# Performance work log

Measured on AMD Instinct MI355X. Metric: run time of the kernel, lower is better.

## Reference

```python
import jax, jax.numpy as jnp
import numpy as np

# --- model config (matches init_kwargs) ---
T, R, L, H, D = 3, 4, 4, 8, 32      # node types, edge types, layers, heads, head dim
HID = H * D                          # hidden = 256
N, E = 16384, 65536                  # nodes per type, edges per edge type
REL = [(1, 0), (0, 2), (2, 1), (0, 0)]  # (src_type, dst_type) per edge type
EPS = 1e-5


def setup_inputs():
    key = jax.random.key(0)
    ks = jax.random.split(key, 24)
    w = lambda k, s: 0.05 * jax.random.normal(k, s, jnp.float32)
    d = {}
    for t in range(T):
        d[f"x{t}"] = jax.random.normal(ks[t], (N, HID), jnp.float32)
    for r in range(R):
        d[f"ei{r}"] = jax.random.randint(ks[3 + r], (2, E), 0, N)
    # input projections (per node type)
    d["Win"] = w(ks[10], (T, HID, HID)); d["b_in"] = jnp.zeros((T, HID), jnp.float32)
    # HGTConv per-layer, per-node-type k/q/v linears
    d["Kw"] = w(ks[11], (L, T, HID, HID)); d["Kb"] = jnp.zeros((L, T, HID), jnp.float32)
    d["Qw"] = w(ks[12], (L, T, HID, HID)); d["Qb"] = jnp.zeros((L, T, HID), jnp.float32)
    d["Vw"] = w(ks[13], (L, T, HID, HID)); d["Vb"] = jnp.zeros((L, T, HID), jnp.float32)
    # per-layer, per-edge-type relation matrices (key/message) and priority
    d["Arel"] = w(ks[14], (L, R, H, D, D)) + jnp.eye(D, dtype=jnp.float32)
    d["Mrel"] = w(ks[15], (L, R, H, D, D)) + jnp.eye(D, dtype=jnp.float32)
    d["Prel"] = jnp.ones((L, R, H), jnp.float32)
    # HGTConv output linear + learned skip gate, encoder LayerNorm
    d["Aw"] = w(ks[16], (L, T, HID, HID)); d["Ab"] = jnp.zeros((L, T, HID), jnp.float32)
    d["skip"] = jnp.ones((L, T), jnp.float32)
    d["ln_g"] = jnp.ones((L, T, HID), jnp.float32); d["ln_b"] = jnp.zeros((L, T, HID), jnp.float32)
    # output projections (per node type)
    d["Wout"] = w(ks[17], (T, HID, HID)); d["b_out"] = jnp.zeros((T, HID), jnp.float32)
    return d


def _layer_norm(y, g, b):
    mu = y.mean(-1, keepdims=True)
    var = ((y - mu) ** 2).mean(-1, keepdims=True)
    return (y - mu) * jax.lax.rsqrt(var + EPS) * g + b


def _hgt_forward(xs, eis, Win, b_in, Kw, Kb, Qw, Qb, Vw, Vb, Arel, Mrel, Prel,
                 Aw, Ab, skip, ln_g, ln_b, Wout, b_out):
    scale = 1.0 / np.sqrt(D).astype(np.float32)
    # input projections (dropout is identity in eval / p=0)
    hs = [xs[t] @ Win[t] + b_in[t] for t in range(T)]
    for l in range(L):
        k = [(hs[t] @ Kw[l, t] + Kb[l, t]).reshape(-1, H, D) for t in range(T)]
        q = [(hs[t] @ Qw[l, t] + Qb[l, t]).reshape(-1, H, D) for t in range(T)]
        v = [(hs[t] @ Vw[l, t] + Vb[l, t]).reshape(-1, H, D) for t in range(T)]
        # per-edge scores / messages, bucketed by destination node type
        sc_by = [[] for _ in range(T)]; mg_by = [[] for _ in range(T)]; di_by = [[] for _ in range(T)]
        for r, (s, dtp) in enumerate(REL):
            src, dst = eis[r][0], eis[r][1]
            k_rel = jnp.einsum('nhd,hde->nhe', k[s], Arel[l, r])  # relation-specific key transform
            m_rel = jnp.einsum('nhd,hde->nhe', v[s], Mrel[l, r])  # relation-specific message transform
            score = jnp.einsum('ehd,ehd->eh', q[dtp][dst], k_rel[src]) * Prel[l, r] * scale  # [E,H]
            sc_by[dtp].append(score); mg_by[dtp].append(m_rel[src]); di_by[dtp].append(dst)
        new_hs = []
        for t in range(T):
            sc = jnp.concatenate(sc_by[t], 0)       # [Et,H] scores over all incoming relations
            mg = jnp.concatenate(mg_by[t], 0)       # [Et,H,D]
            di = jnp.concatenate(di_by[t], 0)       # [Et]
            n = hs[t].shape[0]
            # segment softmax over each destination node's incoming edges (per head)
            mx = jax.ops.segment_max(sc, di, num_segments=n)
            ex = jnp.exp(sc - mx[di])
            den = jax.ops.segment_sum(ex, di, num_segments=n)
            alpha = ex / jnp.maximum(den[di], 1e-16)
            agg = jax.ops.segment_sum(mg * alpha[..., None], di, num_segments=n).reshape(n, HID)
            out = jax.nn.gelu(agg) @ Aw[l, t] + Ab[l, t]
            a = jax.nn.sigmoid(skip[l, t])
            conv = a * out + (1.0 - a) * hs[t]                    # HGTConv internal gated skip
            new_hs.append(_layer_norm(conv + hs[t], ln_g[l, t], ln_b[l, t]))  # encoder residual + LN
        hs = new_hs
    return tuple(hs[t] @ Wout[t] + b_out[t] for t in range(T))


def reference(x0, x1, x2, ei0, ei1, ei2, ei3, Win, b_in, Kw, Kb, Qw, Qb, Vw, Vb,
              Arel, Mrel, Prel, Aw, Ab, skip, ln_g, ln_b, Wout, b_out):
    return _hgt_forward([x0, x1, x2], [ei0, ei1, ei2, ei3], Win, b_in, Kw, Kb, Qw, Qb,
                        Vw, Vb, Arel, Mrel, Prel, Aw, Ab, skip, ln_g, ln_b, Wout, b_out)
```

## Files before the change

kernel.cpp:

```cpp
#include <hip/hip_runtime.h>

#define N_NODES 16384
#define E_EDGES 65536
#define HIDC 256
#define NM ((size_t)N_NODES * HIDC)
#define NSLOT 62
#define PLANEU ((size_t)NSLOT * 65536)
#define KMU ((size_t)N_NODES * 512)

typedef __attribute__((ext_vector_type(8))) short short8;
typedef __attribute__((ext_vector_type(4))) float f32x4;

__device__ __forceinline__ float gelu_f(float x) {
  return 0.5f * x * (1.0f + tanhf(0.7978845608028654f * (x + 0.044715f * x * x * x)));
}
__device__ __forceinline__ unsigned short bf16rne(float x) {
  unsigned u = __float_as_uint(x);
  return (unsigned short)((u + 0x7FFFu + ((u >> 16) & 1u)) >> 16);
}
__device__ __forceinline__ void split2(float x, unsigned short& h, unsigned short& l) {
  h = bf16rne(x);
  float rem = x - __uint_as_float(((unsigned)h) << 16);
  l = bf16rne(rem);
}
__device__ __forceinline__ float bf2f(unsigned short v) {
  return __uint_as_float(((unsigned)v) << 16);
}
__device__ __forceinline__ int src_of(int r) { return (r == 0) ? 1 : (r == 2) ? 2 : 0; }
__device__ __forceinline__ size_t woff(int k, int n) {
  return (size_t)(((n >> 6) & 3) * 16384 + (k >> 5) * 2048 + (((k >> 3) & 3) * 512) + ((n & 63) * 8) + (k & 7));
}
__device__ __forceinline__ size_t swz(int row, int k) {
  return ((size_t)(row >> 4) << 12) + ((size_t)(k >> 3) << 7) + ((row & 15) << 3) + (k & 7);
}

__device__ __forceinline__ void gemm_core(const unsigned short* __restrict__ Ahi,
                                          const unsigned short* __restrict__ Alo,
                                          const unsigned short* __restrict__ Whi,
                                          const unsigned short* __restrict__ Wlo,
                                          int bm, int ntt, f32x4 (&acc)[4][2]) {
  const int tid = threadIdx.x;
  const int w = tid >> 6, l = tid & 63;
  const int wm = (w >> 1) * 64, wn = (w & 1) * 32;
  const int lk = l >> 4, ln = l & 15;
  const size_t abase = ((size_t)((bm + wm) >> 4) << 12) + ln * 8;
  const size_t bbase = (size_t)ntt * 16384 + lk * 512 + (wn + ln) * 8;
  #pragma unroll 2
  for (int ks = 0; ks < 8; ks++) {
    short8 a_h[4], a_l[4], b_h[2], b_l[2];
    #pragma unroll
    for (int mf = 0; mf < 4; mf++) {
      size_t ao = abase + mf * 4096 + (size_t)(ks * 4 + lk) * 128;
      a_h[mf] = *(const short8*)(Ahi + ao);
      a_l[mf] = *(const short8*)(Alo + ao);
    }
    #pragma unroll
    for (int nf = 0; nf < 2; nf++) {
      size_t bo = bbase + ks * 2048 + nf * 128;
      b_h[nf] = *(const short8*)(Whi + bo);
      b_l[nf] = *(const short8*)(Wlo + bo);
    }
    #pragma unroll
    for (int mf = 0; mf < 4; mf++)
      #pragma unroll
      for (int nf = 0; nf < 2; nf++) {
        acc[mf][nf] = __builtin_amdgcn_mfma_f32_16x16x32_bf16(a_l[mf], b_h[nf], acc[mf][nf], 0, 0, 0);
        acc[mf][nf] = __builtin_amdgcn_mfma_f32_16x16x32_bf16(a_h[mf], b_l[nf], acc[mf][nf], 0, 0, 0);
        acc[mf][nf] = __builtin_amdgcn_mfma_f32_16x16x32_bf16(a_h[mf], b_h[nf], acc[mf][nf], 0, 0, 0);
      }
  }
}

__global__ __launch_bounds__(256)
void gemm_layer(int l, const unsigned short* __restrict__ wprep,
                const unsigned short* __restrict__ hsP,
                const float* __restrict__ Qb, const float* __restrict__ fb,
                float* __restrict__ qb3, unsigned short* __restrict__ km) {
  const int y = blockIdx.y;
  const int bm = blockIdx.x * 128;
  const int tid = threadIdx.x;
  const int w = tid >> 6, lx = tid & 63;
  const int wm = (w >> 1) * 64, wn = (w & 1) * 32;
  const int lk = lx >> 4, ln = lx & 15;
  f32x4 acc[4][2];
  #pragma unroll
  for (int a = 0; a < 4; a++)
    #pragma unroll
    for (int b = 0; b < 2; b++) acc[a][b] = f32x4{0.f, 0.f, 0.f, 0.f};

  if (y < 12) {
    const int t = y >> 2, ntt = y & 3;
    const int slot = 3 + l * 3 + t;
    const unsigned short* Ah_ = hsP + (size_t)t * 2 * NM;
    gemm_core(Ah_, Ah_ + NM, wprep + (size_t)slot * 65536, wprep + PLANEU + (size_t)slot * 65536,
              bm, ntt, acc);
    const float* bias = Qb + (l * 3 + t) * 256;
    float* out = qb3 + (size_t)t * NM;
    #pragma unroll
    for (int nf = 0; nf < 2; nf++) {
      const int col = ntt * 64 + wn + nf * 16 + ln;
      const float bv = bias[col];
      #pragma unroll
      for (int mf = 0; mf < 4; mf++) {
        const int row = bm + wm + mf * 16 + lk * 4;
        #pragma unroll
        for (int r4 = 0; r4 < 4; r4++)
          out[(size_t)(row + r4) * HIDC + col] = acc[mf][nf][r4] + bv;
      }
    }
  } else {
    const int y2 = y - 12;
    const int r = y2 >> 3, nt8 = y2 & 7;
    const int lr = l * 4 + r;
    const int s = src_of(r);
    const int slot = 30 + lr * 2 + (nt8 >> 2);
    const int ntt = nt8 & 3;
    const unsigned short* Ah_ = hsP + (size_t)s * 2 * NM;
    gemm_core(Ah_, Ah_ + NM, wprep + (size_t)slot * 65536, wprep + PLANEU + (size_t)slot * 65536,
              bm, ntt, acc);
    unsigned short* kmr = km + (size_t)r * KMU;
    #pragma unroll
    for (int nf = 0; nf < 2; nf++) {
      const int c512 = nt8 * 64 + wn + nf * 16 + ln;
      const float bv = fb[lr * 512 + c512];
      #pragma unroll
      for (int mf = 0; mf < 4; mf++) {
        const int row = bm + wm + mf * 16 + lk * 4;
        #pragma unroll
        for (int r4 = 0; r4 < 4; r4++)
          kmr[(size_t)(row + r4) * 512 + c512] = bf16rne(acc[mf][nf][r4] + bv);
      }
    }
  }
}

template<int OUTM>
__global__ __launch_bounds__(256)
void gemm3(const unsigned short* __restrict__ Abase, const unsigned short* __restrict__ wprep,
           int slot0, const float* __restrict__ bias0,
           float* __restrict__ outf, unsigned short* __restrict__ outP) {
  const int y = blockIdx.y;
  const int t = y >> 2, ntt = y & 3;
  const int bm = blockIdx.x * 128;
  const int tid = threadIdx.x;
  const int w = tid >> 6, lx = tid & 63;
  const int wm = (w >> 1) * 64, wn = (w & 1) * 32;
  const int lk = lx >> 4, ln = lx & 15;
  f32x4 acc[4][2];
  #pragma unroll
  for (int a = 0; a < 4; a++)
    #pragma unroll
    for (int b = 0; b < 2; b++) acc[a][b] = f32x4{0.f, 0.f, 0.f, 0.f};
  const unsigned short* Ah_ = Abase + (size_t)t * 2 * NM;
  const int slot = slot0 + t;
  gemm_core(Ah_, Ah_ + NM, wprep + (size_t)slot * 65536, wprep + PLANEU + (size_t)slot * 65536,
            bm, ntt, acc);
  const float* bias = bias0 + t * 256;
  #pragma unroll
  for (int nf = 0; nf < 2; nf++) {
    const int col = ntt * 64 + wn + nf * 16 + ln;
    const float bv = bias[col];
    #pragma unroll
    for (int mf = 0; mf < 4; mf++) {
      const int row = bm + wm + mf * 16 + lk * 4;
      #pragma unroll
      for (int r4 = 0; r4 < 4; r4++) {
        float val = acc[mf][nf][r4] + bv;
        if (OUTM == 0) {
          outf[(size_t)t * NM + (size_t)(row + r4) * HIDC + col] = val;
        } else if (OUTM == 1) {
          unsigned short h16, l16;
          split2(val, h16, l16);
          size_t o = swz(row + r4, col);
          outP[(size_t)t * 2 * NM + o] = h16;
          outP[(size_t)t * 2 * NM + NM + o] = l16;
        } else {
          outf[(size_t)t * NM + swz(row + r4, col)] = val;
        }
      }
    }
  }
}

__global__ __launch_bounds__(256)
void split_x(const float* __restrict__ x0, const float* __restrict__ x1,
             const float* __restrict__ x2, unsigned short* __restrict__ out) {
  size_t gi = (size_t)blockIdx.x * 2048 + threadIdx.x * 8;
  int t = (int)(gi >> 22);
  size_t i = gi & (NM - 1);
  const float* x = t == 0 ? x0 : t == 1 ? x1 : x2;
  float4 v0 = *(const float4*)(x + i);
  float4 v1 = *(const float4*)(x + i + 4);
  float xs[8] = {v0.x, v0.y, v0.z, v0.w, v1.x, v1.y, v1.z, v1.w};
  short8 h8, l8;
  #pragma unroll
  for (int j = 0; j < 8; j++) {
    unsigned short h, lo;
    split2(xs[j], h, lo);
    h8[j] = (short)h; l8[j] = (short)lo;
  }
  int row = (int)(i >> 8), k = (int)(i & 255);
  size_t o = swz(row, k);
  unsigned short* hp = out + (size_t)t * 2 * NM;
  *(short8*)(hp + o) = h8;
  *(short8*)(hp + NM + o) = l8;
}

__global__ __launch_bounds__(256)
void prep_plain(const float* __restrict__ Win, const float* __restrict__ Qw,
                const float* __restrict__ Aw, const float* __restrict__ Wout,
                unsigned short* __restrict__ wh, unsigned short* __restrict__ wlo) {
  const int j = blockIdx.y;
  const float* src = j < 3  ? Win  + (size_t)j * 65536 :
                     j < 15 ? Qw   + (size_t)(j - 3) * 65536 :
                     j < 27 ? Aw   + (size_t)(j - 15) * 65536 :
                              Wout + (size_t)(j - 27) * 65536;
  const int c = blockIdx.x;
  const int nt = c >> 3, ks = c & 7;
  const int t = threadIdx.x;
  const int n = nt * 64 + (t & 63);
  const int kq = t >> 6;
  const int k = ks * 32 + kq * 8;
  short8 h8, l8;
  #pragma unroll
  for (int i = 0; i < 8; i++) {
    unsigned short h, lo;
    split2(src[(size_t)(k + i) * HIDC + n], h, lo);
    h8[i] = (short)h; l8[i] = (short)lo;
  }
  size_t off = (size_t)j * 65536 + nt * 16384 + ks * 2048 + kq * 512 + (size_t)(t & 63) * 8;
  *(short8*)&wh[off] = h8;
  *(short8*)&wlo[off] = l8;
}

__global__ __launch_bounds__(256)
void fuse_kernel(const float* __restrict__ Kw, const float* __restrict__ Kb,
                 const float* __restrict__ Vw, const float* __restrict__ Vb,
                 const float* __restrict__ Arel, const float* __restrict__ Mrel,
                 unsigned short* __restrict__ wh, unsigned short* __restrict__ wlo,
                 float* __restrict__ fb) {
  const int h = blockIdx.x;
  const int lr = blockIdx.y;
  const int kv = blockIdx.z;
  const int l = lr >> 2, r = lr & 3;
  const int s = src_of(r);
  const float* Wsrc = (kv ? Vw : Kw) + (size_t)(l * 3 + s) * 65536;
  const float* bsrc = (kv ? Vb : Kb) + (size_t)(l * 3 + s) * 256;
  const float* A    = (kv ? Mrel : Arel) + (size_t)lr * 8192 + h * 1024;
  const int slot = 30 + lr * 2 + kv;
  float* fbp = fb + (size_t)lr * 512 + kv * 256;
  __shared__ float Am[32][32];
  const int tid = threadIdx.x;
  #pragma unroll
  for (int i = 0; i < 4; i++) { int p = tid + i * 256; Am[p >> 5][p & 31] = A[p]; }
  __syncthreads();
  float wv[32];
  #pragma unroll
  for (int d = 0; d < 32; d++) wv[d] = Wsrc[(size_t)tid * HIDC + h * 32 + d];
  const size_t sbase = (size_t)slot * 65536;
  #pragma unroll
  for (int e = 0; e < 32; e++) {
    float sacc = 0.0f;
    #pragma unroll
    for (int d = 0; d < 32; d++) sacc += wv[d] * Am[d][e];
    unsigned short hi, lo;
    split2(sacc, hi, lo);
    size_t o = sbase + woff(tid, h * 32 + e);
    wh[o] = hi; wlo[o] = lo;
  }
  if (tid < 32) {
    float sacc = 0.0f;
    #pragma unroll
    for (int d = 0; d < 32; d++) sacc += bsrc[h * 32 + d] * Am[d][tid];
    fbp[h * 32 + tid] = sacc;
  }
}

__global__ __launch_bounds__(256)
void zero_cnt_kernel(int* __restrict__ cnt) {
  cnt[blockIdx.x * 256 + threadIdx.x] = 0;
}
__global__ __launch_bounds__(256)
void count_kernel(const int* __restrict__ e0, const int* __restrict__ e1,
                  const int* __restrict__ e2, const int* __restrict__ e3,
                  int* __restrict__ cnt) {
  int g = blockIdx.x * 256 + threadIdx.x;
  int r = g >> 16, e = g & 0xFFFF;
  const int* ei = (r == 0) ? e0 : (r == 1) ? e1 : (r == 2) ? e2 : e3;
  atomicAdd(&cnt[r * N_NODES + ei[E_EDGES + e]], 1);
}
__global__ __launch_bounds__(256)
void scan_kernel(const int* __restrict__ cnt, int* __restrict__ rp, int* __restrict__ cur) {
  const int r = blockIdx.x;
  const int* c = cnt + r * N_NODES;
  int* rpp = rp + r * (N_NODES + 1);
  int* u = cur + r * N_NODES;
  __shared__ int part[256];
  const int tid = threadIdx.x;
  const int base = tid * 64;
  int s = 0;
  for (int i = 0; i < 64; i++) s += c[base + i];
  part[tid] = s;
  __syncthreads();
  for (int off = 1; off < 256; off <<= 1) {
    int v = (tid >= off) ? part[tid - off] : 0;
    __syncthreads();
    part[tid] += v;
    __syncthreads();
  }
  int run = (tid == 0) ? 0 : part[tid - 1];
  for (int i = 0; i < 64; i++) {
    int idx = base + i;
    rpp[idx] = run;
    u[idx] = run;
    run += c[idx];
  }
  if (tid == 255) rpp[N_NODES] = run;
}
__global__ __launch_bounds__(256)
void fill_kernel(const int* __restrict__ e0, const int* __restrict__ e1,
                 const int* __restrict__ e2, const int* __restrict__ e3,
                 int* __restrict__ cur, int* __restrict__ srcl) {
  int g = blockIdx.x * 256 + threadIdx.x;
  int r = g >> 16, e = g & 0xFFFF;
  const int* ei = (r == 0) ? e0 : (r == 1) ? e1 : (r == 2) ? e2 : e3;
  int pos = atomicAdd(&cur[r * N_NODES + ei[E_EDGES + e]], 1);
  srcl[r * E_EDGES + pos] = ei[e];
}

__global__ __launch_bounds__(256)
void attn_layer(int l, const float* __restrict__ qb3, const unsigned short* __restrict__ km,
                const float* __restrict__ Prel, const int* __restrict__ rp,
                const int* __restrict__ srcl, unsigned short* __restrict__ gp) {
  const int b = blockIdx.x;
  const int t = b >> 12;
  const int n = ((b & 4095) << 2) + (threadIdx.x >> 6);
  const int lane = threadIdx.x & 63;
  const int h = lane >> 3;
  const float scale = 0.17677669529663687f;
  const float* q = qb3 + (size_t)t * NM;
  float4 qv = *(const float4*)(q + (size_t)n * HIDC + lane * 4);
  float m = -INFINITY, den = 0.0f;
  float ax = 0.f, ay = 0.f, az = 0.f, aw = 0.f;

  auto run = [&](int r) {
    const unsigned short* kmr = km + (size_t)r * KMU;
    const float p = Prel[(l * 4 + r) * 8 + h] * scale;
    const int* rpp = rp + r * (N_NODES + 1);
    const int* sl = srcl + r * E_EDGES;
    const int beg = rpp[n], end = rpp[n + 1];
    for (int i = beg; i < end; i++) {
      int src = sl[i];
      const unsigned short* base = kmr + (size_t)src * 512 + lane * 4;
      uint2 uk = *(const uint2*)base;
      uint2 um = *(const uint2*)(base + 256);
      float k0 = __uint_as_float(uk.x << 16), k1 = __uint_as_float(uk.x & 0xFFFF0000u);
      float k2 = __uint_as_float(uk.y << 16), k3 = __uint_as_float(uk.y & 0xFFFF0000u);
      float dot = qv.x * k0 + qv.y * k1 + qv.z * k2 + qv.w * k3;
      dot += __shfl_xor(dot, 1);
      dot += __shfl_xor(dot, 2);
      dot += __shfl_xor(dot, 4);
      float s = dot * p;
      float mn = fmaxf(m, s);
      float c = expf(m - mn);
      float wgt = expf(s - mn);
      den = den * c + wgt;
      float m0 = __uint_as_float(um.x << 16), m1 = __uint_as_float(um.x & 0xFFFF0000u);
      float m2 = __uint_as_float(um.y << 16), m3 = __uint_as_float(um.y & 0xFFFF0000u);
      ax = ax * c + wgt * m0;
      ay = ay * c + wgt * m1;
      az = az * c + wgt * m2;
      aw = aw * c + wgt * m3;
      m = mn;
    }
  };
  if (t == 0) { run(0); run(3); }
  else if (t == 1) { run(2); }
  else { run(1); }

  float inv = 1.0f / fmaxf(den, 1e-16f);
  float vals[4] = {ax * inv, ay * inv, az * inv, aw * inv};
  unsigned short hh[4], ll[4];
  #pragma unroll
  for (int j = 0; j < 4; j++) split2(gelu_f(vals[j]), hh[j], ll[j]);
  unsigned hi01 = (unsigned)hh[0] | ((unsigned)hh[1] << 16);
  unsigned hi23 = (unsigned)hh[2] | ((unsigned)hh[3] << 16);
  unsigned lo01 = (unsigned)ll[0] | ((unsigned)ll[1] << 16);
  unsigned lo23 = (unsigned)ll[2] | ((unsigned)ll[3] << 16);
  unsigned short* oh = gp + (size_t)t * 2 * NM;
  size_t o = ((size_t)(n >> 4) << 12) + ((size_t)(lane >> 1) << 7) + ((n & 15) << 3) + ((lane & 1) << 2);
  *(uint2*)(oh + o) = make_uint2(hi01, hi23);
  *(uint2*)(oh + NM + o) = make_uint2(lo01, lo23);
}

__global__ __launch_bounds__(256)
void ln_layer(int l, const float* __restrict__ qb3s, unsigned short* __restrict__ hsP,
              const float* __restrict__ skipA, const float* __restrict__ ln_g,
              const float* __restrict__ ln_b) {
  const int b = blockIdx.x;
  const int t = b >> 10;
  const int grp = b & 1023;
  const int tid = threadIdx.x;
  const int lt = l * 3 + t;
  const float a = 1.0f / (1.0f + expf(-skipA[lt]));
  unsigned short* hH = hsP + (size_t)t * 2 * NM + (size_t)grp * 4096;
  unsigned short* hL = hH + NM;
  const float* ov = qb3s + (size_t)t * NM + (size_t)grp * 4096;
  float y[16];
  float s = 0.0f;
  #pragma unroll
  for (int j = 0; j < 16; j++) {
    int o = tid + j * 256;
    float hv = bf2f(hH[o]) + bf2f(hL[o]);
    float v = a * ov[o] + (1.0f - a) * hv + hv;
    y[j] = v;
    s += v;
  }
  s += __shfl_xor(s, 1); s += __shfl_xor(s, 2); s += __shfl_xor(s, 4);
  __shared__ float pa[4][8], pb[4][8];
  const int w = tid >> 6, lane = tid & 63;
  if ((lane & 7) == 0) pa[w][lane >> 3] = s;
  __syncthreads();
  const int r = (tid >> 3) & 15;
  float mu = (pa[r >> 3][r & 7] + pa[(r >> 3) + 2][r & 7]) * (1.0f / 256.0f);
  float sq = 0.0f;
  #pragma unroll
  for (int j = 0; j < 16; j++) { float d = y[j] - mu; sq += d * d; }
  sq += __shfl_xor(sq, 1); sq += __shfl_xor(sq, 2); sq += __shfl_xor(sq, 4);
  if ((lane & 7) == 0) pb[w][lane >> 3] = sq;
  __syncthreads();
  float var = (pb[r >> 3][r & 7] + pb[(r >> 3) + 2][r & 7]) * (1.0f / 256.0f);
  float rs = 1.0f / sqrtf(var + 1e-5f);
  const float* gv = ln_g + lt * 256;
  const float* bv = ln_b + lt * 256;
  #pragma unroll
  for (int j = 0; j < 16; j++) {
    int o = tid + j * 256;
    int k = ((tid >> 7) + 2 * j) * 8 + (tid & 7);
    float out = (y[j] - mu) * rs * gv[k] + bv[k];
    unsigned short h16, l16;
    split2(out, h16, l16);
    hH[o] = h16;
    hL[o] = l16;
  }
}

extern "C" void kernel_launch(void* const* d_in, const int* in_sizes, int n_in,
                              void* d_out, int out_size, void* d_ws, size_t ws_size,
                              hipStream_t stream) {
  const float* x0 = (const float*)d_in[0];
  const float* x1 = (const float*)d_in[1];
  const float* x2 = (const float*)d_in[2];
  const int* ei[4] = {(const int*)d_in[3], (const int*)d_in[4], (const int*)d_in[5], (const int*)d_in[6]};
  const float* Win  = (const float*)d_in[7];
  const float* b_in = (const float*)d_in[8];
  const float* Kw   = (const float*)d_in[9];
  const float* Kb   = (const float*)d_in[10];
  const float* Qw   = (const float*)d_in[11];
  const float* Qb   = (const float*)d_in[12];
  const float* Vw   = (const float*)d_in[13];
  const float* Vb   = (const float*)d_in[14];
  const float* Arel = (const float*)d_in[15];
  const float* Mrel = (const float*)d_in[16];
  const float* Prel = (const float*)d_in[17];
  const float* Aw   = (const float*)d_in[18];
  const float* Ab   = (const float*)d_in[19];
  const float* skip = (const float*)d_in[20];
  const float* ln_g = (const float*)d_in[21];
  const float* ln_b = (const float*)d_in[22];
  const float* Wout = (const float*)d_in[23];
  const float* b_out= (const float*)d_in[24];

  float* f = (float*)d_ws;
  unsigned short* hsP = (unsigned short*)f;
  float* qb3 = f + 3 * NM;
  unsigned short* km = (unsigned short*)(f + 6 * NM);
  unsigned short* wprep = (unsigned short*)(f + 10 * NM);
  float* fb = (float*)(wprep + 2 * PLANEU);
  int* ib = (int*)(fb + 8192);
  int* cnt  = ib;
  int* rp   = ib + 4 * N_NODES;
  int* cur  = rp + 4 * (N_NODES + 1);
  int* srcl = cur + 4 * N_NODES;
  unsigned short* gp = (unsigned short*)d_out;

  prep_plain<<<dim3(32, 30), 256, 0, stream>>>(Win, Qw, Aw, Wout, wprep, wprep + PLANEU);
  fuse_kernel<<<dim3(8, 16, 2), 256, 0, stream>>>(Kw, Kb, Vw, Vb, Arel, Mrel,
                                                  wprep, wprep + PLANEU, fb);
  split_x<<<3 * NM / 2048, 256, 0, stream>>>(x0, x1, x2, gp);
  zero_cnt_kernel<<<4 * N_NODES / 256, 256, 0, stream>>>(cnt);
  count_kernel<<<4 * E_EDGES / 256, 256, 0, stream>>>(ei[0], ei[1], ei[2], ei[3], cnt);
  scan_kernel<<<4, 256, 0, stream>>>(cnt, rp, cur);
  fill_kernel<<<4 * E_EDGES / 256, 256, 0, stream>>>(ei[0], ei[1], ei[2], ei[3], cur, srcl);

  gemm3<1><<<dim3(128, 12), 256, 0, stream>>>(gp, wprep, 0, b_in, nullptr, hsP);

  for (int l = 0; l < 4; l++) {
    gemm_layer<<<dim3(128, 44), 256, 0, stream>>>(l, wprep, hsP, Qb, fb, qb3, km);
    attn_layer<<<3 * 4096, 256, 0, stream>>>(l, qb3, km, Prel, rp, srcl, gp);
    gemm3<2><<<dim3(128, 12), 256, 0, stream>>>(gp, wprep, 15 + l * 3, Ab + l * 3 * 256,
                                                qb3, nullptr);
    ln_layer<<<3 * 1024, 256, 0, stream>>>(l, qb3, hsP, skip, ln_g, ln_b);
  }

  gemm3<0><<<dim3(128, 12), 256, 0, stream>>>(hsP, wprep, 27, b_out, (float*)d_out, nullptr);
}
```

Measured before the change: 1.206 ms.

## Stage 64-row A stripes in LDS and compute full 256-wide output per block

The GEMM kernels now load a 64-row stripe of the split bf16 activation (hi and lo) into shared memory once per block. Each 512-thread block then computes all 256 output columns for that stripe, instead of each 256-thread block reading A straight from global memory for a single 64-column tile. This cuts redundant global reads of A, which was fetched once per column tile, and regroups the per-layer K/Q/V blocks by source node type. In exchange it uses 64 KB of LDS per block, which may limit occupancy, and adds a block barrier after staging.

```diff
diff --git a/kernel.cpp b/kernel.cpp
--- a/kernel.cpp
+++ b/kernel.cpp
@@ -34,31 +34,46 @@
   return ((size_t)(row >> 4) << 12) + ((size_t)(k >> 3) << 7) + ((row & 15) << 3) + (k & 7);
 }
 
-__device__ __forceinline__ void gemm_core(const unsigned short* __restrict__ Ahi,
-                                          const unsigned short* __restrict__ Alo,
-                                          const unsigned short* __restrict__ Whi,
-                                          const unsigned short* __restrict__ Wlo,
-                                          int bm, int ntt, f32x4 (&acc)[4][2]) {
+__device__ __forceinline__ void stage_A(const unsigned short* __restrict__ Ahi,
+                                        const unsigned short* __restrict__ Alo,
+                                        int stripe, short* AhS, short* AlS) {
+  const int tid = threadIdx.x;
+  const unsigned short* aH = Ahi + (size_t)stripe * 16384;
+  const unsigned short* aL = Alo + (size_t)stripe * 16384;
+  #pragma unroll
+  for (int rnd = 0; rnd < 4; rnd++) {
+    int idx = rnd * 4096 + tid * 8;
+    *(short8*)&AhS[idx] = *(const short8*)(aH + idx);
+    *(short8*)&AlS[idx] = *(const short8*)(aL + idx);
+  }
+  __syncthreads();
+}
+
+__device__ __forceinline__ void compute_tile(const short* AhS, const short* AlS,
+                                             const unsigned short* __restrict__ Whi,
+                                             const unsigned short* __restrict__ Wlo,
+                                             size_t slotbase, f32x4 (&acc)[4][2]) {
   const int tid = threadIdx.x;
   const int w = tid >> 6, l = tid & 63;
-  const int wm = (w >> 1) * 64, wn = (w & 1) * 32;
+  const int ntt = w >> 1, wn = (w & 1) * 32;
   const int lk = l >> 4, ln = l & 15;
-  const size_t abase = ((size_t)((bm + wm) >> 4) << 12) + ln * 8;
-  const size_t bbase = (size_t)ntt * 16384 + lk * 512 + (wn + ln) * 8;
+  const size_t bbase = slotbase + ntt * 16384 + lk * 512 + (wn + ln) * 8;
+  const int a0 = lk * 128 + ln * 8;
   #pragma unroll 2
   for (int ks = 0; ks < 8; ks++) {
-    short8 a_h[4], a_l[4], b_h[2], b_l[2];
-    #pragma unroll
-    for (int mf = 0; mf < 4; mf++) {
-      size_t ao = abase + mf * 4096 + (size_t)(ks * 4 + lk) * 128;
-      a_h[mf] = *(const short8*)(Ahi + ao);
-      a_l[mf] = *(const short8*)(Alo + ao);
-    }
+    short8 b_h[2], b_l[2];
     #pragma unroll
     for (int nf = 0; nf < 2; nf++) {
       size_t bo = bbase + ks * 2048 + nf * 128;
       b_h[nf] = *(const short8*)(Whi + bo);
       b_l[nf] = *(const short8*)(Wlo + bo);
+    }
+    short8 a_h[4], a_l[4];
+    #pragma unroll
+    for (int mf = 0; mf < 4; mf++) {
+      int ao = mf * 4096 + ks * 512 + a0;
+      a_h[mf] = *(const short8*)&AhS[ao];
+      a_l[mf] = *(const short8*)&AlS[ao];
     }
     #pragma unroll
     for (int mf = 0; mf < 4; mf++)
@@ -71,61 +86,66 @@
   }
 }
 
-__global__ __launch_bounds__(256)
-void gemm_layer(int l, const unsigned short* __restrict__ wprep,
-                const unsigned short* __restrict__ hsP,
-                const float* __restrict__ Qb, const float* __restrict__ fb,
-                float* __restrict__ qb3, unsigned short* __restrict__ km) {
+__global__ __launch_bounds__(512)
+void gemm_src(int l, const unsigned short* __restrict__ wprep,
+              const unsigned short* __restrict__ hsP,
+              const float* __restrict__ Qb, const float* __restrict__ fb,
+              float* __restrict__ qb3, unsigned short* __restrict__ km) {
+  __shared__ short AhS[16384], AlS[16384];
   const int y = blockIdx.y;
-  const int bm = blockIdx.x * 128;
+  const int stripe = blockIdx.x;
+  int s, qt = -1, r = 0, half = 0;
+  if (y == 0)      { s = 0; qt = 0; }
+  else if (y < 5)  { s = 0; r = (y < 3) ? 3 : 1; half = (y == 2) | (y == 4); }
+  else if (y == 5) { s = 1; qt = 1; }
+  else if (y < 8)  { s = 1; r = 0; half = y - 6; }
+  else if (y == 8) { s = 2; qt = 2; }
+  else             { s = 2; r = 2; half = y - 9; }
+
+  const unsigned short* Ah_ = hsP + (size_t)s * 2 * NM;
+  stage_A(Ah_, Ah_ + NM, stripe, AhS, AlS);
+
+  f32x4 acc[4][2];
+  #pragma unroll
+  for (int a = 0; a < 4; a++)
+    #pragma unroll
+    for (int b = 0; b < 2; b++) acc[a][b] = f32x4{0.f, 0.f, 0.f, 0.f};
+
+  const int slot = (qt >= 0) ? (3 + l * 3 + qt) : (30 + (l * 4 + r) * 2 + half);
+  compute_tile(AhS, AlS, wprep, wprep + PLANEU, (size_t)slot * 65536, acc);
+
   const int tid = threadIdx.x;
   const int w = tid >> 6, lx = tid & 63;
-  const int wm = (w >> 1) * 64, wn = (w & 1) * 32;
+  const int ntt = w >> 1, wn = (w & 1) * 32;
   const int lk = lx >> 4, ln = lx & 15;
-  f32x4 acc[4][2];
-  #pragma unroll
-  for (int a = 0; a < 4; a++)
-    #pragma unroll
-    for (int b = 0; b < 2; b++) acc[a][b] = f32x4{0.f, 0.f, 0.f, 0.f};
-
-  if (y < 12) {
-    const int t = y >> 2, ntt = y & 3;
-    const int slot = 3 + l * 3 + t;
-    const unsigned short* Ah_ = hsP + (size_t)t * 2 * NM;
-    gemm_core(Ah_, Ah_ + NM, wprep + (size_t)slot * 65536, wprep + PLANEU + (size_t)slot * 65536,
-              bm, ntt, acc);
-    const float* bias = Qb + (l * 3 + t) * 256;
-    float* out = qb3 + (size_t)t * NM;
+
+  if (qt >= 0) {
+    const float* bias = Qb + (l * 3 + qt) * 256;
+    float* out = qb3 + (size_t)qt * NM;
     #pragma unroll
     for (int nf = 0; nf < 2; nf++) {
       const int col = ntt * 64 + wn + nf * 16 + ln;
       const float bv = bias[col];
       #pragma unroll
       for (int mf = 0; mf < 4; mf++) {
-        const int row = bm + wm + mf * 16 + lk * 4;
+        const int row = stripe * 64 + mf * 16 + lk * 4;
         #pragma unroll
         for (int r4 = 0; r4 < 4; r4++)
           out[(size_t)(row + r4) * HIDC + col] = acc[mf][nf][r4] + bv;
       }
     }
   } else {
-    const int y2 = y - 12;
-    const int r = y2 >> 3, nt8 = y2 & 7;
     const int lr = l * 4 + r;
-    const int s = src_of(r);
-    const int slot = 30 + lr * 2 + (nt8 >> 2);
-    const int ntt = nt8 & 3;
-    const unsigned short* Ah_ = hsP + (size_t)s * 2 * NM;
-    gemm_core(Ah_, Ah_ + NM, wprep + (size_t)slot * 65536, wprep + PLANEU + (size_t)slot * 65536,
-              bm, ntt, acc);
+    const float* bias = fb + lr * 512 + half * 256;
     unsigned short* kmr = km + (size_t)r * KMU;
     #pragma unroll
     for (int nf = 0; nf < 2; nf++) {
-      const int c512 = nt8 * 64 + wn + nf * 16 + ln;
-      const float bv = fb[lr * 512 + c512];
+      const int col = ntt * 64 + wn + nf * 16 + ln;
+      const int c512 = half * 256 + col;
+      const float bv = bias[col];
       #pragma unroll
       for (int mf = 0; mf < 4; mf++) {
-        const int row = bm + wm + mf * 16 + lk * 4;
+        const int row = stripe * 64 + mf * 16 + lk * 4;
         #pragma unroll
         for (int r4 = 0; r4 < 4; r4++)
           kmr[(size_t)(row + r4) * 512 + c512] = bf16rne(acc[mf][nf][r4] + bv);
@@ -135,26 +155,27 @@
 }
 
 template<int OUTM>
-__global__ __launch_bounds__(256)
-void gemm3(const unsigned short* __restrict__ Abase, const unsigned short* __restrict__ wprep,
-           int slot0, const float* __restrict__ bias0,
-           float* __restrict__ outf, unsigned short* __restrict__ outP) {
-  const int y = blockIdx.y;
-  const int t = y >> 2, ntt = y & 3;
-  const int bm = blockIdx.x * 128;
+__global__ __launch_bounds__(512)
+void gemm3_s(const unsigned short* __restrict__ Abase, const unsigned short* __restrict__ wprep,
+             int slot0, const float* __restrict__ bias0,
+             float* __restrict__ outf, unsigned short* __restrict__ outP) {
+  __shared__ short AhS[16384], AlS[16384];
+  const int t = blockIdx.y;
+  const int stripe = blockIdx.x;
+  const unsigned short* Ah_ = Abase + (size_t)t * 2 * NM;
+  stage_A(Ah_, Ah_ + NM, stripe, AhS, AlS);
+
+  f32x4 acc[4][2];
+  #pragma unroll
+  for (int a = 0; a < 4; a++)
+    #pragma unroll
+    for (int b = 0; b < 2; b++) acc[a][b] = f32x4{0.f, 0.f, 0.f, 0.f};
+  compute_tile(AhS, AlS, wprep, wprep + PLANEU, (size_t)(slot0 + t) * 65536, acc);
+
   const int tid = threadIdx.x;
   const int w = tid >> 6, lx = tid & 63;
-  const int wm = (w >> 1) * 64, wn = (w & 1) * 32;
+  const int ntt = w >> 1, wn = (w & 1) * 32;
   const int lk = lx >> 4, ln = lx & 15;
-  f32x4 acc[4][2];
-  #pragma unroll
-  for (int a = 0; a < 4; a++)
-    #pragma unroll
-    for (int b = 0; b < 2; b++) acc[a][b] = f32x4{0.f, 0.f, 0.f, 0.f};
-  const unsigned short* Ah_ = Abase + (size_t)t * 2 * NM;
-  const int slot = slot0 + t;
-  gemm_core(Ah_, Ah_ + NM, wprep + (size_t)slot * 65536, wprep + PLANEU + (size_t)slot * 65536,
-            bm, ntt, acc);
   const float* bias = bias0 + t * 256;
   #pragma unroll
   for (int nf = 0; nf < 2; nf++) {
@@ -162,7 +183,7 @@
     const float bv = bias[col];
     #pragma unroll
     for (int mf = 0; mf < 4; mf++) {
-      const int row = bm + wm + mf * 16 + lk * 4;
+      const int row = stripe * 64 + mf * 16 + lk * 4;
       #pragma unroll
       for (int r4 = 0; r4 < 4; r4++) {
         float val = acc[mf][nf][r4] + bv;
@@ -493,15 +514,15 @@
   scan_kernel<<<4, 256, 0, stream>>>(cnt, rp, cur);
   fill_kernel<<<4 * E_EDGES / 256, 256, 0, stream>>>(ei[0], ei[1], ei[2], ei[3], cur, srcl);
 
-  gemm3<1><<<dim3(128, 12), 256, 0, stream>>>(gp, wprep, 0, b_in, nullptr, hsP);
+  gemm3_s<1><<<dim3(256, 3), 512, 0, stream>>>(gp, wprep, 0, b_in, nullptr, hsP);
 
   for (int l = 0; l < 4; l++) {
-    gemm_layer<<<dim3(128, 44), 256, 0, stream>>>(l, wprep, hsP, Qb, fb, qb3, km);
+    gemm_src<<<dim3(256, 11), 512, 0, stream>>>(l, wprep, hsP, Qb, fb, qb3, km);
     attn_layer<<<3 * 4096, 256, 0, stream>>>(l, qb3, km, Prel, rp, srcl, gp);
-    gemm3<2><<<dim3(128, 12), 256, 0, stream>>>(gp, wprep, 15 + l * 3, Ab + l * 3 * 256,
-                                                qb3, nullptr);
+    gemm3_s<2><<<dim3(256, 3), 512, 0, stream>>>(gp, wprep, 15 + l * 3, Ab + l * 3 * 256,
+                                                 qb3, nullptr);
     ln_layer<<<3 * 1024, 256, 0, stream>>>(l, qb3, hsP, skip, ln_g, ln_b);
   }
 
-  gemm3<0><<<dim3(128, 12), 256, 0, stream>>>(hsP, wprep, 27, b_out, (float*)d_out, nullptr);
-}
+  gemm3_s<0><<<dim3(256, 3), 512, 0, stream>>>(hsP, wprep, 27, b_out, (float*)d_out, nullptr);
+}
```

After: 1.067 ms. 11.6% less time.
